# Optimization experiments

Measured on AMD Instinct MI355X. Metric: run time of the kernel, lower is better.

Reference implementation:

```python
import jax, jax.numpy as jnp
import numpy as np

EPS_NORM = 1e-12   # F.normalize eps
EPS_SQRT = 1e-8    # epsilon inside sqrt for l2


def setup_inputs() -> dict:
    key = jax.random.key(0)
    k1, k2 = jax.random.split(key)
    B, N, P, D = 8, 16384, 512, 64
    x = jax.random.normal(k1, (B, N, D), dtype=jnp.float32)
    prototypes = jax.random.normal(k2, (P, D), dtype=jnp.float32)
    return {"x": x, "prototypes": prototypes}


def reference(x, prototypes):
    # L2-normalize prototypes (torch.nn.functional.normalize, p=2, dim=-1)
    pnorm = jnp.linalg.norm(prototypes, axis=-1, keepdims=True)
    p = prototypes / jnp.maximum(pnorm, EPS_NORM)            # (P, D)

    x2 = jnp.sum(x * x, axis=-1)                             # (B, N)
    p2 = jnp.sum(p * p, axis=-1)                             # (P,)
    xp = jnp.einsum('bnd,pd->bnp', x, p)                     # (B, N, P)
    sq = x2[..., None] - 2.0 * xp + p2[None, None, :]
    sq = jnp.maximum(sq, 0.0)
    distances = jnp.sqrt(sq + EPS_SQRT)                      # (B, N, P)

    # topk(k=1, largest=False) over dim=-2 (the patch dim N)
    prototype_dist = jnp.min(distances, axis=-2)             # (B, P)
    patches_idcs = jnp.argmin(distances, axis=-2)            # (B, P)
    return prototype_dist, patches_idcs
```

## Files before the change

kernel.cpp:

```cpp
#include <hip/hip_runtime.h>
#include <math.h>

constexpr int B = 8, N = 16384, P = 512, D = 64;
constexpr int NSPLIT   = 16;
constexpr int ROWS_PB  = N / NSPLIT;
constexpr int CHUNK    = 128;
constexpr int NCHUNK   = ROWS_PB / CHUNK;
constexpr int TPB      = 256;

typedef __attribute__((ext_vector_type(8))) _Float16 f16x8;
typedef __attribute__((ext_vector_type(4))) float f32x4;
typedef __attribute__((ext_vector_type(4))) int   i32x4;
using u32 = unsigned int;
using u64 = unsigned long long;

constexpr int X2S   = 65536;
constexpr int P2S   = 69632;
constexpr int PLO   = 70656;
constexpr int SMEMB = 103424;

__device__ __forceinline__ void cvt2(float a, float b, u32& hw, u32& lw) {
    _Float16 ha = (_Float16)a, hb = (_Float16)b;
    float ra = a - (float)ha, rb = b - (float)hb;
    _Float16 la = (_Float16)ra, lb = (_Float16)rb;
    hw = (u32)__builtin_bit_cast(unsigned short, ha) |
         ((u32)__builtin_bit_cast(unsigned short, hb) << 16);
    lw = (u32)__builtin_bit_cast(unsigned short, la) |
         ((u32)__builtin_bit_cast(unsigned short, lb) << 16);
}

__global__ __launch_bounds__(1024, 4)
void kmain(const float* __restrict__ x, const float* __restrict__ proto,
           u64* __restrict__ pk) {
    __shared__ __align__(16) char smem[SMEMB];
    const int t  = threadIdx.x;
    const int l  = t & 63;
    const int wv = t >> 6;
    const int wr = wv >> 2, wc = wv & 3;
    const int hi = l >> 4, il = l & 15;
    const int ns = blockIdx.x, pt = blockIdx.y, b = blockIdx.z;
    const int n0  = ns * ROWS_PB;
    const int pt0 = pt * TPB;

    if (t < TPB) {
        const float4* pr4 = reinterpret_cast<const float4*>(proto + (size_t)(pt0 + t) * D);
        float a0 = 0.f, a1 = 0.f, a2 = 0.f, a3 = 0.f;
        float4 v[16];
        #pragma unroll
        for (int i = 0; i < 16; ++i) {
            v[i] = pr4[i];
            a0 = fmaf(v[i].x, v[i].x, a0);
            a1 = fmaf(v[i].y, v[i].y, a1);
            a2 = fmaf(v[i].z, v[i].z, a2);
            a3 = fmaf(v[i].w, v[i].w, a3);
        }
        float nrm = sqrtf((a0 + a1) + (a2 + a3));
        float sc  = 1.0f / fmaxf(nrm, 1e-12f);
        char* prow = smem + t * 272;
        char* plor = smem + PLO + t * 128;
        int psw = (t & 7) << 4;
        float q0 = 0.f, q1 = 0.f, q2 = 0.f, q3 = 0.f;
        #pragma unroll
        for (int g = 0; g < 8; ++g) {
            float4 va = v[2 * g], vb = v[2 * g + 1];
            float e[8] = {va.x * sc, va.y * sc, va.z * sc, va.w * sc,
                          vb.x * sc, vb.y * sc, vb.z * sc, vb.w * sc};
            q0 = fmaf(e[0], e[0], fmaf(e[4], e[4], q0));
            q1 = fmaf(e[1], e[1], fmaf(e[5], e[5], q1));
            q2 = fmaf(e[2], e[2], fmaf(e[6], e[6], q2));
            q3 = fmaf(e[3], e[3], fmaf(e[7], e[7], q3));
            u32 H[4], Lo[4];
            #pragma unroll
            for (int jj = 0; jj < 4; ++jj)
                cvt2(e[2 * jj], e[2 * jj + 1], H[jj], Lo[jj]);
            *reinterpret_cast<i32x4*>(prow + g * 16) = i32x4{(int)H[0], (int)H[1], (int)H[2], (int)H[3]};
            *reinterpret_cast<i32x4*>(plor + ((g * 16) ^ psw)) = i32x4{(int)Lo[0], (int)Lo[1], (int)Lo[2], (int)Lo[3]};
        }
        *reinterpret_cast<float*>(smem + P2S + t * 4) = (q0 + q1) + (q2 + q3);
    }
    __syncthreads();

    f16x8 bh[2][4];
    #pragma unroll
    for (int s = 0; s < 2; ++s)
        #pragma unroll
        for (int ni = 0; ni < 4; ++ni) {
            int row = wc * 64 + ni * 16 + il;
            bh[s][ni] = *reinterpret_cast<const f16x8*>(smem + row * 272 + s * 64 + hi * 16);
        }
    float p2c[4];
    #pragma unroll
    for (int ni = 0; ni < 4; ++ni)
        p2c[ni] = *reinterpret_cast<const float*>(smem + P2S + (wc * 64 + ni * 16 + il) * 4);
    __syncthreads();

    const int alow  = (hi * 16) ^ ((il & 3) << 4);
    const int abit6 = (il & 4) << 4;
    const int rowbase = (wr * 32 + il) * 256 + alow;
    const int blbase  = PLO + (wc * 64 + il) * 128 + alow;

    const float* gx = x + ((size_t)b * N + n0) * D + t * 8;

    auto stage = [&](int c, int buf) {
        const float4* src = reinterpret_cast<const float4*>(gx + (size_t)c * CHUNK * D);
        float4 L0 = src[0], L1 = src[1];
        float vals[8] = {L0.x, L0.y, L0.z, L0.w, L1.x, L1.y, L1.z, L1.w};
        float s8 = 0.f;
        #pragma unroll
        for (int i = 0; i < 8; ++i) s8 = fmaf(vals[i], vals[i], s8);
        s8 += __shfl_xor(s8, 1);
        s8 += __shfl_xor(s8, 2);
        s8 += __shfl_xor(s8, 4);
        int row = t >> 3, oct = t & 7;
        if (oct == 0) *reinterpret_cast<float*>(smem + X2S + buf * 512 + row * 4) = s8;
        char* base = smem + buf * 32768 + row * 256;
        int ob = (oct * 16) ^ ((row & 7) << 4);
        u32 H[4], Lo[4];
        #pragma unroll
        for (int jj = 0; jj < 4; ++jj)
            cvt2(vals[2 * jj], vals[2 * jj + 1], H[jj], Lo[jj]);
        *reinterpret_cast<i32x4*>(base +       ob) = i32x4{(int)H[0], (int)H[1], (int)H[2], (int)H[3]};
        *reinterpret_cast<i32x4*>(base + 128 + ob) = i32x4{(int)Lo[0], (int)Lo[1], (int)Lo[2], (int)Lo[3]};
    };

    stage(0, 0);
    __syncthreads();

    float msq[4]  = {3.4e38f, 3.4e38f, 3.4e38f, 3.4e38f};
    int   midx[4] = {0, 0, 0, 0};

    for (int c = 0; c < NCHUNK; ++c) {
        const int buf = c & 1;
        f32x4 acc[2][4];
        #pragma unroll
        for (int mi = 0; mi < 2; ++mi)
            #pragma unroll
            for (int ni = 0; ni < 4; ++ni) acc[mi][ni] = f32x4{0.f, 0.f, 0.f, 0.f};

        const int bufo = buf * 32768;
        #pragma unroll
        for (int s = 0; s < 2; ++s) {
            const int soff = (s * 64) ^ abit6;
            f16x8 ah[2], al[2], blv[4];
            #pragma unroll
            for (int mi = 0; mi < 2; ++mi) {
                ah[mi] = *reinterpret_cast<const f16x8*>(smem + bufo + rowbase + mi * 4096 + soff);
                al[mi] = *reinterpret_cast<const f16x8*>(smem + bufo + rowbase + mi * 4096 + 128 + soff);
            }
            #pragma unroll
            for (int ni = 0; ni < 4; ++ni)
                blv[ni] = *reinterpret_cast<const f16x8*>(smem + blbase + ni * 2048 + soff);
            #pragma unroll
            for (int mi = 0; mi < 2; ++mi)
                #pragma unroll
                for (int ni = 0; ni < 4; ++ni) {
                    acc[mi][ni] = __builtin_amdgcn_mfma_f32_16x16x32_f16(
                        ah[mi], bh[s][ni], acc[mi][ni], 0, 0, 0);
                    acc[mi][ni] = __builtin_amdgcn_mfma_f32_16x16x32_f16(
                        ah[mi], blv[ni], acc[mi][ni], 0, 0, 0);
                    acc[mi][ni] = __builtin_amdgcn_mfma_f32_16x16x32_f16(
                        al[mi], bh[s][ni], acc[mi][ni], 0, 0, 0);
                }
        }

        const float* x2p = reinterpret_cast<const float*>(smem + X2S + buf * 512);
        const int idxb = n0 + c * CHUNK + wr * 32 + hi * 4;
        #pragma unroll
        for (int mi = 0; mi < 2; ++mi) {
            f32x4 xv = *reinterpret_cast<const f32x4*>(x2p + wr * 32 + mi * 16 + hi * 4);
            #pragma unroll
            for (int ni = 0; ni < 4; ++ni) {
                #pragma unroll
                for (int r = 0; r < 4; ++r) {
                    float sq = fmaf(-2.0f, acc[mi][ni][r], xv[r] + p2c[ni]);
                    sq = fmaxf(sq, 0.0f);
                    int idx = idxb + mi * 16 + r;
                    if (sq < msq[ni]) { msq[ni] = sq; midx[ni] = idx; }
                }
            }
        }

        if (c + 1 < NCHUNK) stage(c + 1, buf ^ 1);
        __syncthreads();
    }

    u64 key[4];
    #pragma unroll
    for (int ni = 0; ni < 4; ++ni) {
        u64 k = ((u64)__float_as_uint(msq[ni]) << 32) | (u32)midx[ni];
        u64 o = __shfl_xor(k, 16); k = o < k ? o : k;
        o     = __shfl_xor(k, 32); k = o < k ? o : k;
        key[ni] = k;
    }
    u64* xch = reinterpret_cast<u64*>(smem);
    if (wr > 0 && l < 16) {
        #pragma unroll
        for (int ni = 0; ni < 4; ++ni)
            xch[(wr - 1) * 256 + wc * 64 + ni * 16 + l] = key[ni];
    }
    __syncthreads();
    if (wr == 0 && l < 16) {
        #pragma unroll
        for (int ni = 0; ni < 4; ++ni) {
            u64 kk = key[ni];
            #pragma unroll
            for (int q = 0; q < 3; ++q) {
                u64 o = xch[q * 256 + wc * 64 + ni * 16 + l];
                kk = o < kk ? o : kk;
            }
            pk[(size_t)ns * (B * P) + (size_t)b * P + pt0 + wc * 64 + ni * 16 + l] = kk;
        }
    }
}

__global__ void kfin(const u64* __restrict__ pk, float* __restrict__ out) {
    int i = blockIdx.x * 256 + threadIdx.x;
    if (i >= B * P) return;
    u64 m = pk[i];
    #pragma unroll
    for (int s = 1; s < NSPLIT; ++s) {
        u64 c = pk[(size_t)s * (B * P) + i];
        m = c < m ? c : m;
    }
    float sq = __uint_as_float((u32)(m >> 32));
    out[i] = sqrtf(sq + 1e-8f);
    out[B * P + i] = (float)(u32)(m & 0xFFFFFFFFu);
}

extern "C" void kernel_launch(void* const* d_in, const int* in_sizes, int n_in,
                              void* d_out, int out_size, void* d_ws, size_t ws_size,
                              hipStream_t stream) {
    const float* x     = (const float*)d_in[0];
    const float* proto = (const float*)d_in[1];
    float* out = (float*)d_out;
    u64* pk = (u64*)d_ws;

    kmain<<<dim3(NSPLIT, P / TPB, B), dim3(1024), 0, stream>>>(x, proto, pk);
    kfin<<<dim3((B * P + 255) / 256), dim3(256), 0, stream>>>(pk, out);
}
```

Before: 106.0 us.

## Keep prototype fragments in LDS and prefetch next x chunk before epilogue

Prototype hi/lo fragments are no longer held in registers. Both halves now live in one swizzled 256-byte-per-row LDS region and are reloaded inside the main loop, which frees registers and one barrier. The global load of the next x chunk is issued right after the MFMAs and before the min/argmin epilogue, so its latency overlaps compute. The first chunk's load is hoisted above the prototype normalization. LDS usage grows to about 130KB and LDS read traffic per iteration rises.

After: 97.96 us. 1.08x faster.

```diff
diff --git a/kernel.cpp b/kernel.cpp
--- a/kernel.cpp
+++ b/kernel.cpp
@@ -14,10 +14,10 @@
 using u32 = unsigned int;
 using u64 = unsigned long long;
 
-constexpr int X2S   = 65536;
-constexpr int P2S   = 69632;
-constexpr int PLO   = 70656;
-constexpr int SMEMB = 103424;
+constexpr int BREG  = 65536;
+constexpr int X2S   = 131072;
+constexpr int P2S   = 132096;
+constexpr int SMEMB = 133120;
 
 __device__ __forceinline__ void cvt2(float a, float b, u32& hw, u32& lw) {
     _Float16 ha = (_Float16)a, hb = (_Float16)b;
@@ -42,6 +42,14 @@
     const int n0  = ns * ROWS_PB;
     const int pt0 = pt * TPB;
 
+    const float* gxbase = x + ((size_t)b * N + n0) * D;
+    const int srow = t >> 3, soct = t & 7;
+    float4 A0, A1;
+    {
+        const float4* src = reinterpret_cast<const float4*>(gxbase) + t * 2;
+        A0 = src[0]; A1 = src[1];
+    }
+
     if (t < TPB) {
         const float4* pr4 = reinterpret_cast<const float4*>(proto + (size_t)(pt0 + t) * D);
         float a0 = 0.f, a1 = 0.f, a2 = 0.f, a3 = 0.f;
@@ -56,8 +64,7 @@
         }
         float nrm = sqrtf((a0 + a1) + (a2 + a3));
         float sc  = 1.0f / fmaxf(nrm, 1e-12f);
-        char* prow = smem + t * 272;
-        char* plor = smem + PLO + t * 128;
+        char* prow = smem + BREG + t * 256;
         int psw = (t & 7) << 4;
         float q0 = 0.f, q1 = 0.f, q2 = 0.f, q3 = 0.f;
         #pragma unroll
@@ -73,37 +80,14 @@
             #pragma unroll
             for (int jj = 0; jj < 4; ++jj)
                 cvt2(e[2 * jj], e[2 * jj + 1], H[jj], Lo[jj]);
-            *reinterpret_cast<i32x4*>(prow + g * 16) = i32x4{(int)H[0], (int)H[1], (int)H[2], (int)H[3]};
-            *reinterpret_cast<i32x4*>(plor + ((g * 16) ^ psw)) = i32x4{(int)Lo[0], (int)Lo[1], (int)Lo[2], (int)Lo[3]};
+            int ob = (g * 16) ^ psw;
+            *reinterpret_cast<i32x4*>(prow +       ob) = i32x4{(int)H[0], (int)H[1], (int)H[2], (int)H[3]};
+            *reinterpret_cast<i32x4*>(prow + 128 + ob) = i32x4{(int)Lo[0], (int)Lo[1], (int)Lo[2], (int)Lo[3]};
         }
         *reinterpret_cast<float*>(smem + P2S + t * 4) = (q0 + q1) + (q2 + q3);
     }
-    __syncthreads();
-
-    f16x8 bh[2][4];
-    #pragma unroll
-    for (int s = 0; s < 2; ++s)
-        #pragma unroll
-        for (int ni = 0; ni < 4; ++ni) {
-            int row = wc * 64 + ni * 16 + il;
-            bh[s][ni] = *reinterpret_cast<const f16x8*>(smem + row * 272 + s * 64 + hi * 16);
-        }
-    float p2c[4];
-    #pragma unroll
-    for (int ni = 0; ni < 4; ++ni)
-        p2c[ni] = *reinterpret_cast<const float*>(smem + P2S + (wc * 64 + ni * 16 + il) * 4);
-    __syncthreads();
-
-    const int alow  = (hi * 16) ^ ((il & 3) << 4);
-    const int abit6 = (il & 4) << 4;
-    const int rowbase = (wr * 32 + il) * 256 + alow;
-    const int blbase  = PLO + (wc * 64 + il) * 128 + alow;
-
-    const float* gx = x + ((size_t)b * N + n0) * D + t * 8;
-
-    auto stage = [&](int c, int buf) {
-        const float4* src = reinterpret_cast<const float4*>(gx + (size_t)c * CHUNK * D);
-        float4 L0 = src[0], L1 = src[1];
+
+    auto stage_write = [&](float4 L0, float4 L1, int buf) {
         float vals[8] = {L0.x, L0.y, L0.z, L0.w, L1.x, L1.y, L1.z, L1.w};
         float s8 = 0.f;
         #pragma unroll
@@ -111,10 +95,9 @@
         s8 += __shfl_xor(s8, 1);
         s8 += __shfl_xor(s8, 2);
         s8 += __shfl_xor(s8, 4);
-        int row = t >> 3, oct = t & 7;
-        if (oct == 0) *reinterpret_cast<float*>(smem + X2S + buf * 512 + row * 4) = s8;
-        char* base = smem + buf * 32768 + row * 256;
-        int ob = (oct * 16) ^ ((row & 7) << 4);
+        if (soct == 0) *reinterpret_cast<float*>(smem + X2S + buf * 512 + srow * 4) = s8;
+        char* base = smem + buf * 32768 + srow * 256;
+        int ob = (soct * 16) ^ ((srow & 7) << 4);
         u32 H[4], Lo[4];
         #pragma unroll
         for (int jj = 0; jj < 4; ++jj)
@@ -123,44 +106,77 @@
         *reinterpret_cast<i32x4*>(base + 128 + ob) = i32x4{(int)Lo[0], (int)Lo[1], (int)Lo[2], (int)Lo[3]};
     };
 
-    stage(0, 0);
+    stage_write(A0, A1, 0);
     __syncthreads();
+
+    const int alow  = (hi * 16) ^ ((il & 3) << 4);
+    const int abit6 = (il & 4) << 4;
+    int arow[2];
+    #pragma unroll
+    for (int mi = 0; mi < 2; ++mi)
+        arow[mi] = (wr * 32 + mi * 16 + il) * 256 + alow;
+    int brow[4];
+    #pragma unroll
+    for (int ni = 0; ni < 4; ++ni)
+        brow[ni] = BREG + (wc * 64 + ni * 16 + il) * 256 + alow;
+
+    float p2c[4];
+    #pragma unroll
+    for (int ni = 0; ni < 4; ++ni)
+        p2c[ni] = *reinterpret_cast<const float*>(
+            smem + P2S + (wc * 64 + ni * 16 + il) * 4);
 
     float msq[4]  = {3.4e38f, 3.4e38f, 3.4e38f, 3.4e38f};
     int   midx[4] = {0, 0, 0, 0};
 
     for (int c = 0; c < NCHUNK; ++c) {
         const int buf = c & 1;
+        const int bufo = buf * 32768;
         f32x4 acc[2][4];
         #pragma unroll
         for (int mi = 0; mi < 2; ++mi)
             #pragma unroll
             for (int ni = 0; ni < 4; ++ni) acc[mi][ni] = f32x4{0.f, 0.f, 0.f, 0.f};
 
-        const int bufo = buf * 32768;
         #pragma unroll
         for (int s = 0; s < 2; ++s) {
             const int soff = (s * 64) ^ abit6;
-            f16x8 ah[2], al[2], blv[4];
+            f16x8 ah[2], al[2], bh[4], bl[4];
             #pragma unroll
             for (int mi = 0; mi < 2; ++mi) {
-                ah[mi] = *reinterpret_cast<const f16x8*>(smem + bufo + rowbase + mi * 4096 + soff);
-                al[mi] = *reinterpret_cast<const f16x8*>(smem + bufo + rowbase + mi * 4096 + 128 + soff);
+                ah[mi] = *reinterpret_cast<const f16x8*>(smem + bufo + arow[mi] + soff);
+                al[mi] = *reinterpret_cast<const f16x8*>(smem + bufo + arow[mi] + 128 + soff);
             }
             #pragma unroll
             for (int ni = 0; ni < 4; ++ni)
-                blv[ni] = *reinterpret_cast<const f16x8*>(smem + blbase + ni * 2048 + soff);
-            #pragma unroll
-            for (int mi = 0; mi < 2; ++mi)
-                #pragma unroll
-                for (int ni = 0; ni < 4; ++ni) {
+                bh[ni] = *reinterpret_cast<const f16x8*>(smem + brow[ni] + soff);
+            #pragma unroll
+            for (int ni = 0; ni < 4; ++ni)
+                #pragma unroll
+                for (int mi = 0; mi < 2; ++mi)
                     acc[mi][ni] = __builtin_amdgcn_mfma_f32_16x16x32_f16(
-                        ah[mi], bh[s][ni], acc[mi][ni], 0, 0, 0);
+                        ah[mi], bh[ni], acc[mi][ni], 0, 0, 0);
+            #pragma unroll
+            for (int ni = 0; ni < 4; ++ni)
+                #pragma unroll
+                for (int mi = 0; mi < 2; ++mi)
                     acc[mi][ni] = __builtin_amdgcn_mfma_f32_16x16x32_f16(
-                        ah[mi], blv[ni], acc[mi][ni], 0, 0, 0);
+                        al[mi], bh[ni], acc[mi][ni], 0, 0, 0);
+            #pragma unroll
+            for (int ni = 0; ni < 4; ++ni)
+                bl[ni] = *reinterpret_cast<const f16x8*>(smem + brow[ni] + 128 + soff);
+            #pragma unroll
+            for (int ni = 0; ni < 4; ++ni)
+                #pragma unroll
+                for (int mi = 0; mi < 2; ++mi)
                     acc[mi][ni] = __builtin_amdgcn_mfma_f32_16x16x32_f16(
-                        al[mi], bh[s][ni], acc[mi][ni], 0, 0, 0);
-                }
+                        ah[mi], bl[ni], acc[mi][ni], 0, 0, 0);
+        }
+
+        if (c + 1 < NCHUNK) {
+            const float4* src = reinterpret_cast<const float4*>(
+                gxbase + (size_t)(c + 1) * CHUNK * D) + t * 2;
+            A0 = src[0]; A1 = src[1];
         }
 
         const float* x2p = reinterpret_cast<const float*>(smem + X2S + buf * 512);
@@ -180,7 +196,7 @@
             }
         }
 
-        if (c + 1 < NCHUNK) stage(c + 1, buf ^ 1);
+        if (c + 1 < NCHUNK) stage_write(A0, A1, buf ^ 1);
         __syncthreads();
     }
 
```
